# Performance work log

Hardware: AMD Instinct MI355X
Metric: run time of the kernel (lower is better)

## Reference

```python
import jax, jax.numpy as jnp
import numpy as np

NUM_SRC = 100000
NUM_DST = 100000
NUM_EDGES = 800000
WIDTH = 128
LEAKY_SLOPE = 0.01  # torch LeakyReLU default


def setup_inputs() -> dict:
    key = jax.random.key(0)
    k1, k2, k3, k4 = jax.random.split(key, 4)
    x_src = jax.random.normal(k1, (NUM_SRC, WIDTH), dtype=jnp.float32)
    x_dst = jax.random.normal(k2, (NUM_DST, WIDTH), dtype=jnp.float32)
    e = jax.random.randint(k3, (2, NUM_EDGES), 0, NUM_DST, dtype=jnp.int64)
    W = jax.random.normal(k4, (2 * WIDTH, WIDTH), dtype=jnp.float32) * 0.02
    b = jnp.zeros((WIDTH,), dtype=jnp.float32)
    return {"x_src": x_src, "x_dst": x_dst, "e": e, "W": W, "b": b}


def reference(x_src, x_dst, e, W, b):
    src_idx, dst_idx = e[0], e[1]
    # gather + per-edge diff: [E, W]
    diffs = x_dst[dst_idx] - x_src[src_idx]
    # segment max over destination nodes; empty segments -> 0 (matches torch.zeros_like init)
    seg_max = jax.ops.segment_max(diffs, dst_idx, num_segments=NUM_DST)
    counts = jax.ops.segment_sum(jnp.ones((diffs.shape[0],), dtype=x_dst.dtype),
                                 dst_idx, num_segments=NUM_DST)
    maxes = jnp.where(counts[:, None] > 0, seg_max, jnp.zeros_like(seg_max))
    # MLP: Linear(2W -> W) + LeakyReLU, then residual
    h = jnp.concatenate([x_dst, maxes], axis=1) @ W + b
    h = jax.nn.leaky_relu(h, negative_slope=LEAKY_SLOPE)
    return x_dst + h
```

## Files before the change

### kernel.cpp

```cpp
#include <hip/hip_runtime.h>

#define WIDTH 128
#define SLOPE 0.01f
#define FBM 64

typedef __attribute__((ext_vector_type(8))) short short8;
typedef __attribute__((ext_vector_type(4))) float f32x4;

__device__ __forceinline__ unsigned short f2bf(float f) {
    unsigned b = __float_as_uint(f);
    b += 0x7FFFu + ((b >> 16) & 1u);
    return (unsigned short)(b >> 16);
}
__device__ __forceinline__ float4 upk(uint2 u) {
    float4 r;
    r.x = __uint_as_float(u.x << 16);
    r.y = __uint_as_float(u.x & 0xFFFF0000u);
    r.z = __uint_as_float(u.y << 16);
    r.w = __uint_as_float(u.y & 0xFFFF0000u);
    return r;
}
__device__ __forceinline__ float4 fmin4(float4 a, float4 b) {
    return make_float4(fminf(a.x, b.x), fminf(a.y, b.y),
                       fminf(a.z, b.z), fminf(a.w, b.w));
}
__device__ __forceinline__ int swz(int lr, int bc) {
    return lr * 512 + (bc ^ ((lr & 7) << 4));
}

__global__ void prep_kernel(const float* __restrict__ x_src,
                            const float* __restrict__ W,
                            const int* __restrict__ e,
                            unsigned short* __restrict__ xsb,
                            unsigned short* __restrict__ Wt,
                            unsigned* __restrict__ counts,
                            int* __restrict__ rank,
                            int NS, int E, int nconv, int nhist) {
    int b = blockIdx.x;
    if (b < nconv) {
        int i = b * 256 + threadIdx.x;
        if (i < NS * 32) {
            float4 v = reinterpret_cast<const float4*>(x_src)[i];
            ushort4 o;
            o.x = f2bf(v.x); o.y = f2bf(v.y); o.z = f2bf(v.z); o.w = f2bf(v.w);
            *reinterpret_cast<ushort4*>(xsb + (size_t)i * 4) = o;
        }
    } else if (b < nconv + nhist) {
        int i = (b - nconv) * 256 + threadIdx.x;
        if (i < E) {
            int dst = e[E + i];
            rank[i] = (int)atomicAdd(&counts[dst], 1u);
        }
    } else {
        int t = (b - nconv - nhist) * 256 + threadIdx.x;
        if (t < 128 * 64) {
            int n = t & 127, kc = t >> 7;
            ushort4 o;
            unsigned short* op = &o.x;
            #pragma unroll
            for (int j = 0; j < 4; ++j) {
                int k = kc * 4 + j;
                float v;
                if (k < 128) v = W[(size_t)k * 128 + n] + W[(size_t)(k + 128) * 128 + n];
                else         v = -W[(size_t)k * 128 + n];
                op[j] = f2bf(v);
            }
            *reinterpret_cast<ushort4*>(Wt + (size_t)n * 256 + kc * 4) = o;
        }
    }
}

__global__ void __launch_bounds__(512) scanA_kernel(
        const unsigned* __restrict__ counts,
        int* __restrict__ loffs,
        unsigned* __restrict__ bsums, int M) {
    int t = threadIdx.x;
    int i = blockIdx.x * 512 + t;
    unsigned c = (i < M) ? counts[i] : 0u;
    unsigned v = c;
    int lane = t & 63, w = t >> 6;
    #pragma unroll
    for (int d = 1; d < 64; d <<= 1) {
        unsigned n = __shfl_up(v, d);
        if (lane >= d) v += n;
    }
    __shared__ unsigned ws[8];
    if (lane == 63) ws[w] = v;
    __syncthreads();
    unsigned wb = 0;
    for (int k = 0; k < w; ++k) wb += ws[k];
    if (i < M) loffs[i] = (int)(wb + v - c);
    if (t == 511) bsums[blockIdx.x] = wb + v;
}

__global__ void scanB_kernel(const unsigned* __restrict__ bsums,
                             int* __restrict__ bbase, int NB) {
    __shared__ unsigned s[256];
    int t = threadIdx.x;
    unsigned v = (t < NB) ? bsums[t] : 0u;
    s[t] = v;
    __syncthreads();
    for (int off = 1; off < 256; off <<= 1) {
        unsigned n = (t >= off) ? s[t - off] : 0u;
        __syncthreads();
        s[t] += n;
        __syncthreads();
    }
    if (t < NB) bbase[t] = (int)(s[t] - v);
}

__global__ void scatter_kernel(const int* __restrict__ e,
                               const int* __restrict__ loffs,
                               const int* __restrict__ bbase,
                               const int* __restrict__ rank,
                               int* __restrict__ csr, int E) {
    int i = blockIdx.x * blockDim.x + threadIdx.x;
    if (i < E) {
        int dst = e[E + i];
        csr[loffs[dst] + bbase[dst >> 9] + rank[i]] = e[i];
    }
}

template<int XSB>
__device__ __forceinline__ void gstep(const float* xs_f,
                                      const unsigned short* xs_b,
                                      const int* csr, int p, int lim,
                                      int half, int cl, float4& mn) {
    int i0 = csr[min(p + 0, lim)];
    int i1 = csr[min(p + 1, lim)];
    int i2 = csr[min(p + 2, lim)];
    int i3 = csr[min(p + 3, lim)];
    int i4 = csr[min(p + 4, lim)];
    int i5 = csr[min(p + 5, lim)];
    int i6 = csr[min(p + 6, lim)];
    int i7 = csr[min(p + 7, lim)];
    int a0 = half ? i1 : i0;
    int a1 = half ? i3 : i2;
    int a2 = half ? i5 : i4;
    int a3 = half ? i7 : i6;
    float4 w0, w1, w2, w3;
    if (XSB) {
        uint2 u0 = *reinterpret_cast<const uint2*>(xs_b + (size_t)a0 * 128 + cl * 4);
        uint2 u1 = *reinterpret_cast<const uint2*>(xs_b + (size_t)a1 * 128 + cl * 4);
        uint2 u2 = *reinterpret_cast<const uint2*>(xs_b + (size_t)a2 * 128 + cl * 4);
        uint2 u3 = *reinterpret_cast<const uint2*>(xs_b + (size_t)a3 * 128 + cl * 4);
        w0 = upk(u0); w1 = upk(u1); w2 = upk(u2); w3 = upk(u3);
    } else {
        const float4* xs4 = reinterpret_cast<const float4*>(xs_f);
        w0 = xs4[(size_t)a0 * 32 + cl];
        w1 = xs4[(size_t)a1 * 32 + cl];
        w2 = xs4[(size_t)a2 * 32 + cl];
        w3 = xs4[(size_t)a3 * 32 + cl];
    }
    mn = fmin4(mn, fmin4(fmin4(w0, w1), fmin4(w2, w3)));
}

template<int XSB>
__global__ __launch_bounds__(256, 4) void fused_kernel(
        const float* __restrict__ x_src,
        const unsigned short* __restrict__ xsb,
        const float* __restrict__ x_dst,
        const int* __restrict__ loffs,
        const int* __restrict__ bbase,
        const int* __restrict__ csr,
        const unsigned short* __restrict__ Wt,
        const float* __restrict__ bias,
        float* __restrict__ out, int M, int E) {
    __shared__ unsigned short At[FBM * 256];
    char* Ab = reinterpret_cast<char*>(At);
    int tid = threadIdx.x;
    int lane = tid & 63;
    int wv = tid >> 6;
    int blockRow = blockIdx.x * FBM;

    #pragma unroll
    for (int i = 0; i < 8; ++i) {
        int u = tid + 256 * i;
        int lr = u >> 5;
        int c4 = u & 31;
        int gr = min(blockRow + lr, M - 1);
        float4 v = reinterpret_cast<const float4*>(x_dst)[(size_t)gr * 32 + c4];
        ushort4 o;
        o.x = f2bf(v.x); o.y = f2bf(v.y); o.z = f2bf(v.z); o.w = f2bf(v.w);
        *reinterpret_cast<ushort4*>(Ab + swz(lr, c4 * 8)) = o;
    }
    __syncthreads();

    int half = lane >> 5, cl = lane & 31;
    for (int j = 0; j < 4; ++j) {
        int lrb = wv * 16 + 4 * j;
        int beg0, beg1, beg2, beg3, end0, end1, end2, end3;
        {
            int r = __builtin_amdgcn_readfirstlane(blockRow + lrb);
            int g[5];
            #pragma unroll
            for (int k = 0; k < 5; ++k) {
                int x = r + k;
                g[k] = (x < M) ? (loffs[x] + bbase[x >> 9]) : E;
            }
            beg0 = (r + 0 < M) ? g[0] : 0;  end0 = (r + 0 < M) ? g[1] : 0;
            beg1 = (r + 1 < M) ? g[1] : 0;  end1 = (r + 1 < M) ? g[2] : 0;
            beg2 = (r + 2 < M) ? g[2] : 0;  end2 = (r + 2 < M) ? g[3] : 0;
            beg3 = (r + 3 < M) ? g[3] : 0;  end3 = (r + 3 < M) ? g[4] : 0;
        }
        float4 mn0 = make_float4(INFINITY, INFINITY, INFINITY, INFINITY);
        float4 mn1 = mn0, mn2 = mn0, mn3 = mn0;
        int p0 = beg0, p1 = beg1, p2 = beg2, p3 = beg3;
        while ((p0 < end0) | (p1 < end1) | (p2 < end2) | (p3 < end3)) {
            if (p0 < end0) { gstep<XSB>(x_src, xsb, csr, p0, end0 - 1, half, cl, mn0); p0 += 8; }
            if (p1 < end1) { gstep<XSB>(x_src, xsb, csr, p1, end1 - 1, half, cl, mn1); p1 += 8; }
            if (p2 < end2) { gstep<XSB>(x_src, xsb, csr, p2, end2 - 1, half, cl, mn2); p2 += 8; }
            if (p3 < end3) { gstep<XSB>(x_src, xsb, csr, p3, end3 - 1, half, cl, mn3); p3 += 8; }
        }
        mn0.x = fminf(mn0.x, __shfl_xor(mn0.x, 32));
        mn0.y = fminf(mn0.y, __shfl_xor(mn0.y, 32));
        mn0.z = fminf(mn0.z, __shfl_xor(mn0.z, 32));
        mn0.w = fminf(mn0.w, __shfl_xor(mn0.w, 32));
        mn1.x = fminf(mn1.x, __shfl_xor(mn1.x, 32));
        mn1.y = fminf(mn1.y, __shfl_xor(mn1.y, 32));
        mn1.z = fminf(mn1.z, __shfl_xor(mn1.z, 32));
        mn1.w = fminf(mn1.w, __shfl_xor(mn1.w, 32));
        mn2.x = fminf(mn2.x, __shfl_xor(mn2.x, 32));
        mn2.y = fminf(mn2.y, __shfl_xor(mn2.y, 32));
        mn2.z = fminf(mn2.z, __shfl_xor(mn2.z, 32));
        mn2.w = fminf(mn2.w, __shfl_xor(mn2.w, 32));
        mn3.x = fminf(mn3.x, __shfl_xor(mn3.x, 32));
        mn3.y = fminf(mn3.y, __shfl_xor(mn3.y, 32));
        mn3.z = fminf(mn3.z, __shfl_xor(mn3.z, 32));
        mn3.w = fminf(mn3.w, __shfl_xor(mn3.w, 32));

        {
            int lr = lrb + half;
            bool has = half ? (end1 > beg1) : (end0 > beg0);
            float4 m = half ? mn1 : mn0;
            ushort4 o;
            if (has) {
                o.x = f2bf(m.x); o.y = f2bf(m.y); o.z = f2bf(m.z); o.w = f2bf(m.w);
            } else {
                o = *reinterpret_cast<const ushort4*>(Ab + swz(lr, cl * 8));
            }
            *reinterpret_cast<ushort4*>(Ab + swz(lr, 256 + cl * 8)) = o;
        }
        {
            int lr = lrb + 2 + half;
            bool has = half ? (end3 > beg3) : (end2 > beg2);
            float4 m = half ? mn3 : mn2;
            ushort4 o;
            if (has) {
                o.x = f2bf(m.x); o.y = f2bf(m.y); o.z = f2bf(m.z); o.w = f2bf(m.w);
            } else {
                o = *reinterpret_cast<const ushort4*>(Ab + swz(lr, cl * 8));
            }
            *reinterpret_cast<ushort4*>(Ab + swz(lr, 256 + cl * 8)) = o;
        }
    }
    __syncthreads();

    int l15 = lane & 15;
    int q = lane >> 4;
    int ncol0 = wv * 32;

    f32x4 acc[4][2];
    #pragma unroll
    for (int t = 0; t < 4; ++t) {
        acc[t][0] = (f32x4){0.f, 0.f, 0.f, 0.f};
        acc[t][1] = (f32x4){0.f, 0.f, 0.f, 0.f};
    }
    size_t b0off = (size_t)(ncol0 + l15) * 256;
    size_t b1off = (size_t)(ncol0 + 16 + l15) * 256;

    #pragma unroll
    for (int s = 0; s < 8; ++s) {
        int koff = s * 32 + q * 8;
        short8 b0 = *reinterpret_cast<const short8*>(Wt + b0off + koff);
        short8 b1 = *reinterpret_cast<const short8*>(Wt + b1off + koff);
        #pragma unroll
        for (int t = 0; t < 4; ++t) {
            int lr = t * 16 + l15;
            short8 a = *reinterpret_cast<const short8*>(Ab + swz(lr, koff * 2));
            acc[t][0] = __builtin_amdgcn_mfma_f32_16x16x32_bf16(b0, a, acc[t][0], 0, 0, 0);
            acc[t][1] = __builtin_amdgcn_mfma_f32_16x16x32_bf16(b1, a, acc[t][1], 0, 0, 0);
        }
    }

    float4 bi[2];
    bi[0] = *reinterpret_cast<const float4*>(bias + ncol0 + q * 4);
    bi[1] = *reinterpret_cast<const float4*>(bias + ncol0 + 16 + q * 4);
    #pragma unroll
    for (int t = 0; t < 4; ++t) {
        int lr = t * 16 + l15;
        int row = blockRow + lr;
        if (row < M) {
            #pragma unroll
            for (int u = 0; u < 2; ++u) {
                int col = ncol0 + u * 16 + q * 4;
                uint2 xu = *reinterpret_cast<const uint2*>(Ab + swz(lr, col * 2));
                float4 xb = upk(xu);
                float4 o;
                float h;
                h = acc[t][u][0] + bi[u].x; o.x = xb.x + (h > 0.f ? h : SLOPE * h);
                h = acc[t][u][1] + bi[u].y; o.y = xb.y + (h > 0.f ? h : SLOPE * h);
                h = acc[t][u][2] + bi[u].z; o.z = xb.z + (h > 0.f ? h : SLOPE * h);
                h = acc[t][u][3] + bi[u].w; o.w = xb.w + (h > 0.f ? h : SLOPE * h);
                *reinterpret_cast<float4*>(out + (size_t)row * 128 + col) = o;
            }
        }
    }
}

extern "C" void kernel_launch(void* const* d_in, const int* in_sizes, int n_in,
                              void* d_out, int out_size, void* d_ws, size_t ws_size,
                              hipStream_t stream) {
    const float* x_src = (const float*)d_in[0];
    const float* x_dst = (const float*)d_in[1];
    const int*   e     = (const int*)d_in[2];
    const float* W     = (const float*)d_in[3];
    const float* bias  = (const float*)d_in[4];
    float* out = (float*)d_out;

    int NS = in_sizes[0] / WIDTH;
    int E  = in_sizes[2] / 2;
    int M  = in_sizes[1] / WIDTH;
    int NB = (M + 511) / 512;

    unsigned short* xsb = (unsigned short*)d_ws;
    unsigned short* Wt  = xsb + (size_t)NS * WIDTH;
    unsigned* counts  = (unsigned*)(Wt + 128 * 256);
    int*      loffs   = (int*)(counts + M);
    int*      rank    = loffs + M;
    int*      csr     = rank + E;
    unsigned* bsums   = (unsigned*)(csr + E);
    int*      bbase   = (int*)(bsums + NB);
    size_t need = (char*)(bbase + NB) - (char*)d_ws;
    int use_xsb = (ws_size >= need) ? 1 : 0;
    if (!use_xsb) {
        Wt = (unsigned short*)d_ws;
        counts  = (unsigned*)(Wt + 128 * 256);
        loffs   = (int*)(counts + M);
        rank    = loffs + M;
        csr     = rank + E;
        bsums   = (unsigned*)(csr + E);
        bbase   = (int*)(bsums + NB);
    }

    hipMemsetAsync(counts, 0, (size_t)M * sizeof(unsigned), stream);

    int nconv = use_xsb ? (NS * 32 + 255) / 256 : 0;
    int nhist = (E + 255) / 256;
    int nwt   = (128 * 64 + 255) / 256;
    prep_kernel<<<nconv + nhist + nwt, 256, 0, stream>>>(x_src, W, e, xsb, Wt,
                                                         counts, rank, NS, E,
                                                         nconv, nhist);
    scanA_kernel<<<NB, 512, 0, stream>>>(counts, loffs, bsums, M);
    scanB_kernel<<<1, 256, 0, stream>>>(bsums, bbase, NB);
    scatter_kernel<<<(E + 255) / 256, 256, 0, stream>>>(e, loffs, bbase, rank,
                                                        csr, E);

    int fblocks = (M + FBM - 1) / FBM;
    if (use_xsb)
        fused_kernel<1><<<fblocks, 256, 0, stream>>>(x_src, xsb, x_dst, loffs,
                                                     bbase, csr, Wt, bias, out,
                                                     M, E);
    else
        fused_kernel<0><<<fblocks, 256, 0, stream>>>(x_src, xsb, x_dst, loffs,
                                                     bbase, csr, Wt, bias, out,
                                                     M, E);
}
```

Measured before the change: 138.9 us.

## Use order-mapped bf16 packed u16 min for gather and halve row tile

The bf16 copy of x_src is now stored in an order-preserving unsigned encoding. The segment min can then use v_pk_min_u16 on the packed data without unpacking to float, and the encoding is undone once per row. The fused kernel's row tile drops from 64 to 32, with launch bounds raised to 8 blocks per CU, to give more independent gather work and higher occupancy. Row bounds checks are removed, which assumes M is a multiple of the tile size. The fp32 fallback path becomes a simple per-row loop.

Result: faster. 132.5 us (-4.6%).

```diff
diff --git a/kernel.cpp b/kernel.cpp
--- a/kernel.cpp
+++ b/kernel.cpp
@@ -2,7 +2,7 @@
 
 #define WIDTH 128
 #define SLOPE 0.01f
-#define FBM 64
+#define FBM 32
 
 typedef __attribute__((ext_vector_type(8))) short short8;
 typedef __attribute__((ext_vector_type(4))) float f32x4;
@@ -20,9 +20,16 @@
     r.w = __uint_as_float(u.y & 0xFFFF0000u);
     return r;
 }
-__device__ __forceinline__ float4 fmin4(float4 a, float4 b) {
-    return make_float4(fminf(a.x, b.x), fminf(a.y, b.y),
-                       fminf(a.z, b.z), fminf(a.w, b.w));
+__device__ __forceinline__ unsigned short map16(unsigned short x) {
+    return (x & 0x8000u) ? (unsigned short)(~x) : (unsigned short)(x | 0x8000u);
+}
+__device__ __forceinline__ unsigned short unmap16(unsigned u) {
+    return (unsigned short)((u & 0x8000u) ? (u ^ 0x8000u) : (~u & 0xFFFFu));
+}
+__device__ __forceinline__ unsigned pkmin(unsigned a, unsigned b) {
+    unsigned r;
+    asm("v_pk_min_u16 %0, %1, %2" : "=v"(r) : "v"(a), "v"(b));
+    return r;
 }
 __device__ __forceinline__ int swz(int lr, int bc) {
     return lr * 512 + (bc ^ ((lr & 7) << 4));
@@ -42,7 +49,8 @@
         if (i < NS * 32) {
             float4 v = reinterpret_cast<const float4*>(x_src)[i];
             ushort4 o;
-            o.x = f2bf(v.x); o.y = f2bf(v.y); o.z = f2bf(v.z); o.w = f2bf(v.w);
+            o.x = map16(f2bf(v.x)); o.y = map16(f2bf(v.y));
+            o.z = map16(f2bf(v.z)); o.w = map16(f2bf(v.w));
             *reinterpret_cast<ushort4*>(xsb + (size_t)i * 4) = o;
         }
     } else if (b < nconv + nhist) {
@@ -121,11 +129,10 @@
     }
 }
 
-template<int XSB>
-__device__ __forceinline__ void gstep(const float* xs_f,
-                                      const unsigned short* xs_b,
-                                      const int* csr, int p, int lim,
-                                      int half, int cl, float4& mn) {
+__device__ __forceinline__ void gstepm(const unsigned short* __restrict__ xs_b,
+                                       const int* __restrict__ csr,
+                                       int p, int lim,
+                                       int half, int cl, uint2& mn) {
     int i0 = csr[min(p + 0, lim)];
     int i1 = csr[min(p + 1, lim)];
     int i2 = csr[min(p + 2, lim)];
@@ -138,25 +145,18 @@
     int a1 = half ? i3 : i2;
     int a2 = half ? i5 : i4;
     int a3 = half ? i7 : i6;
-    float4 w0, w1, w2, w3;
-    if (XSB) {
-        uint2 u0 = *reinterpret_cast<const uint2*>(xs_b + (size_t)a0 * 128 + cl * 4);
-        uint2 u1 = *reinterpret_cast<const uint2*>(xs_b + (size_t)a1 * 128 + cl * 4);
-        uint2 u2 = *reinterpret_cast<const uint2*>(xs_b + (size_t)a2 * 128 + cl * 4);
-        uint2 u3 = *reinterpret_cast<const uint2*>(xs_b + (size_t)a3 * 128 + cl * 4);
-        w0 = upk(u0); w1 = upk(u1); w2 = upk(u2); w3 = upk(u3);
-    } else {
-        const float4* xs4 = reinterpret_cast<const float4*>(xs_f);
-        w0 = xs4[(size_t)a0 * 32 + cl];
-        w1 = xs4[(size_t)a1 * 32 + cl];
-        w2 = xs4[(size_t)a2 * 32 + cl];
-        w3 = xs4[(size_t)a3 * 32 + cl];
-    }
-    mn = fmin4(mn, fmin4(fmin4(w0, w1), fmin4(w2, w3)));
+    uint2 u0 = *reinterpret_cast<const uint2*>(xs_b + (size_t)a0 * 128 + cl * 4);
+    uint2 u1 = *reinterpret_cast<const uint2*>(xs_b + (size_t)a1 * 128 + cl * 4);
+    uint2 u2 = *reinterpret_cast<const uint2*>(xs_b + (size_t)a2 * 128 + cl * 4);
+    uint2 u3 = *reinterpret_cast<const uint2*>(xs_b + (size_t)a3 * 128 + cl * 4);
+    u0.x = pkmin(u0.x, u1.x); u0.y = pkmin(u0.y, u1.y);
+    u2.x = pkmin(u2.x, u3.x); u2.y = pkmin(u2.y, u3.y);
+    mn.x = pkmin(mn.x, pkmin(u0.x, u2.x));
+    mn.y = pkmin(mn.y, pkmin(u0.y, u2.y));
 }
 
 template<int XSB>
-__global__ __launch_bounds__(256, 4) void fused_kernel(
+__global__ __launch_bounds__(256, 8) void fused_kernel(
         const float* __restrict__ x_src,
         const unsigned short* __restrict__ xsb,
         const float* __restrict__ x_dst,
@@ -174,12 +174,11 @@
     int blockRow = blockIdx.x * FBM;
 
     #pragma unroll
-    for (int i = 0; i < 8; ++i) {
+    for (int i = 0; i < 4; ++i) {
         int u = tid + 256 * i;
         int lr = u >> 5;
         int c4 = u & 31;
-        int gr = min(blockRow + lr, M - 1);
-        float4 v = reinterpret_cast<const float4*>(x_dst)[(size_t)gr * 32 + c4];
+        float4 v = reinterpret_cast<const float4*>(x_dst)[(size_t)(blockRow + lr) * 32 + c4];
         ushort4 o;
         o.x = f2bf(v.x); o.y = f2bf(v.y); o.z = f2bf(v.z); o.w = f2bf(v.w);
         *reinterpret_cast<ushort4*>(Ab + swz(lr, c4 * 8)) = o;
@@ -187,8 +186,8 @@
     __syncthreads();
 
     int half = lane >> 5, cl = lane & 31;
-    for (int j = 0; j < 4; ++j) {
-        int lrb = wv * 16 + 4 * j;
+    for (int j = 0; j < 2; ++j) {
+        int lrb = wv * 8 + 4 * j;
         int beg0, beg1, beg2, beg3, end0, end1, end2, end3;
         {
             int r = __builtin_amdgcn_readfirstlane(blockRow + lrb);
@@ -198,60 +197,80 @@
                 int x = r + k;
                 g[k] = (x < M) ? (loffs[x] + bbase[x >> 9]) : E;
             }
-            beg0 = (r + 0 < M) ? g[0] : 0;  end0 = (r + 0 < M) ? g[1] : 0;
-            beg1 = (r + 1 < M) ? g[1] : 0;  end1 = (r + 1 < M) ? g[2] : 0;
-            beg2 = (r + 2 < M) ? g[2] : 0;  end2 = (r + 2 < M) ? g[3] : 0;
-            beg3 = (r + 3 < M) ? g[3] : 0;  end3 = (r + 3 < M) ? g[4] : 0;
-        }
-        float4 mn0 = make_float4(INFINITY, INFINITY, INFINITY, INFINITY);
-        float4 mn1 = mn0, mn2 = mn0, mn3 = mn0;
-        int p0 = beg0, p1 = beg1, p2 = beg2, p3 = beg3;
-        while ((p0 < end0) | (p1 < end1) | (p2 < end2) | (p3 < end3)) {
-            if (p0 < end0) { gstep<XSB>(x_src, xsb, csr, p0, end0 - 1, half, cl, mn0); p0 += 8; }
-            if (p1 < end1) { gstep<XSB>(x_src, xsb, csr, p1, end1 - 1, half, cl, mn1); p1 += 8; }
-            if (p2 < end2) { gstep<XSB>(x_src, xsb, csr, p2, end2 - 1, half, cl, mn2); p2 += 8; }
-            if (p3 < end3) { gstep<XSB>(x_src, xsb, csr, p3, end3 - 1, half, cl, mn3); p3 += 8; }
-        }
-        mn0.x = fminf(mn0.x, __shfl_xor(mn0.x, 32));
-        mn0.y = fminf(mn0.y, __shfl_xor(mn0.y, 32));
-        mn0.z = fminf(mn0.z, __shfl_xor(mn0.z, 32));
-        mn0.w = fminf(mn0.w, __shfl_xor(mn0.w, 32));
-        mn1.x = fminf(mn1.x, __shfl_xor(mn1.x, 32));
-        mn1.y = fminf(mn1.y, __shfl_xor(mn1.y, 32));
-        mn1.z = fminf(mn1.z, __shfl_xor(mn1.z, 32));
-        mn1.w = fminf(mn1.w, __shfl_xor(mn1.w, 32));
-        mn2.x = fminf(mn2.x, __shfl_xor(mn2.x, 32));
-        mn2.y = fminf(mn2.y, __shfl_xor(mn2.y, 32));
-        mn2.z = fminf(mn2.z, __shfl_xor(mn2.z, 32));
-        mn2.w = fminf(mn2.w, __shfl_xor(mn2.w, 32));
-        mn3.x = fminf(mn3.x, __shfl_xor(mn3.x, 32));
-        mn3.y = fminf(mn3.y, __shfl_xor(mn3.y, 32));
-        mn3.z = fminf(mn3.z, __shfl_xor(mn3.z, 32));
-        mn3.w = fminf(mn3.w, __shfl_xor(mn3.w, 32));
-
-        {
-            int lr = lrb + half;
-            bool has = half ? (end1 > beg1) : (end0 > beg0);
-            float4 m = half ? mn1 : mn0;
-            ushort4 o;
-            if (has) {
-                o.x = f2bf(m.x); o.y = f2bf(m.y); o.z = f2bf(m.z); o.w = f2bf(m.w);
-            } else {
-                o = *reinterpret_cast<const ushort4*>(Ab + swz(lr, cl * 8));
-            }
-            *reinterpret_cast<ushort4*>(Ab + swz(lr, 256 + cl * 8)) = o;
-        }
-        {
-            int lr = lrb + 2 + half;
-            bool has = half ? (end3 > beg3) : (end2 > beg2);
-            float4 m = half ? mn3 : mn2;
-            ushort4 o;
-            if (has) {
-                o.x = f2bf(m.x); o.y = f2bf(m.y); o.z = f2bf(m.z); o.w = f2bf(m.w);
-            } else {
-                o = *reinterpret_cast<const ushort4*>(Ab + swz(lr, cl * 8));
-            }
-            *reinterpret_cast<ushort4*>(Ab + swz(lr, 256 + cl * 8)) = o;
+            beg0 = g[0]; end0 = g[1];
+            beg1 = g[1]; end1 = g[2];
+            beg2 = g[2]; end2 = g[3];
+            beg3 = g[3]; end3 = g[4];
+        }
+        if (XSB) {
+            uint2 mn0 = make_uint2(~0u, ~0u);
+            uint2 mn1 = mn0, mn2 = mn0, mn3 = mn0;
+            int p0 = beg0, p1 = beg1, p2 = beg2, p3 = beg3;
+            while ((p0 < end0) | (p1 < end1) | (p2 < end2) | (p3 < end3)) {
+                if (p0 < end0) { gstepm(xsb, csr, p0, end0 - 1, half, cl, mn0); p0 += 8; }
+                if (p1 < end1) { gstepm(xsb, csr, p1, end1 - 1, half, cl, mn1); p1 += 8; }
+                if (p2 < end2) { gstepm(xsb, csr, p2, end2 - 1, half, cl, mn2); p2 += 8; }
+                if (p3 < end3) { gstepm(xsb, csr, p3, end3 - 1, half, cl, mn3); p3 += 8; }
+            }
+            mn0.x = pkmin(mn0.x, (unsigned)__shfl_xor((int)mn0.x, 32));
+            mn0.y = pkmin(mn0.y, (unsigned)__shfl_xor((int)mn0.y, 32));
+            mn1.x = pkmin(mn1.x, (unsigned)__shfl_xor((int)mn1.x, 32));
+            mn1.y = pkmin(mn1.y, (unsigned)__shfl_xor((int)mn1.y, 32));
+            mn2.x = pkmin(mn2.x, (unsigned)__shfl_xor((int)mn2.x, 32));
+            mn2.y = pkmin(mn2.y, (unsigned)__shfl_xor((int)mn2.y, 32));
+            mn3.x = pkmin(mn3.x, (unsigned)__shfl_xor((int)mn3.x, 32));
+            mn3.y = pkmin(mn3.y, (unsigned)__shfl_xor((int)mn3.y, 32));
+
+            {
+                int lr = lrb + half;
+                bool has = half ? (end1 > beg1) : (end0 > beg0);
+                uint2 m;
+                m.x = half ? mn1.x : mn0.x;
+                m.y = half ? mn1.y : mn0.y;
+                ushort4 o;
+                if (has) {
+                    o.x = unmap16(m.x & 0xFFFFu); o.y = unmap16(m.x >> 16);
+                    o.z = unmap16(m.y & 0xFFFFu); o.w = unmap16(m.y >> 16);
+                } else {
+                    o = *reinterpret_cast<const ushort4*>(Ab + swz(lr, cl * 8));
+                }
+                *reinterpret_cast<ushort4*>(Ab + swz(lr, 256 + cl * 8)) = o;
+            }
+            {
+                int lr = lrb + 2 + half;
+                bool has = half ? (end3 > beg3) : (end2 > beg2);
+                uint2 m;
+                m.x = half ? mn3.x : mn2.x;
+                m.y = half ? mn3.y : mn2.y;
+                ushort4 o;
+                if (has) {
+                    o.x = unmap16(m.x & 0xFFFFu); o.y = unmap16(m.x >> 16);
+                    o.z = unmap16(m.y & 0xFFFFu); o.w = unmap16(m.y >> 16);
+                } else {
+                    o = *reinterpret_cast<const ushort4*>(Ab + swz(lr, cl * 8));
+                }
+                *reinterpret_cast<ushort4*>(Ab + swz(lr, 256 + cl * 8)) = o;
+            }
+        } else {
+            const float2* xf = reinterpret_cast<const float2*>(x_src);
+            #pragma unroll
+            for (int k = 0; k < 4; ++k) {
+                int lr = lrb + k;
+                int rb = (k == 0) ? beg0 : (k == 1) ? beg1 : (k == 2) ? beg2 : beg3;
+                int re = (k == 0) ? end0 : (k == 1) ? end1 : (k == 2) ? end2 : end3;
+                float2 mf = make_float2(INFINITY, INFINITY);
+                for (int p = rb; p < re; ++p) {
+                    int idx = csr[p];
+                    float2 v = xf[(size_t)idx * 64 + lane];
+                    mf.x = fminf(mf.x, v.x); mf.y = fminf(mf.y, v.y);
+                }
+                unsigned o;
+                if (re > rb)
+                    o = (unsigned)f2bf(mf.x) | ((unsigned)f2bf(mf.y) << 16);
+                else
+                    o = *reinterpret_cast<const unsigned*>(Ab + swz(lr, lane * 4));
+                *reinterpret_cast<unsigned*>(Ab + swz(lr, 256 + lane * 4)) = o;
+            }
         }
     }
     __syncthreads();
@@ -260,9 +279,9 @@
     int q = lane >> 4;
     int ncol0 = wv * 32;
 
-    f32x4 acc[4][2];
-    #pragma unroll
-    for (int t = 0; t < 4; ++t) {
+    f32x4 acc[2][2];
+    #pragma unroll
+    for (int t = 0; t < 2; ++t) {
         acc[t][0] = (f32x4){0.f, 0.f, 0.f, 0.f};
         acc[t][1] = (f32x4){0.f, 0.f, 0.f, 0.f};
     }
@@ -275,7 +294,7 @@
         short8 b0 = *reinterpret_cast<const short8*>(Wt + b0off + koff);
         short8 b1 = *reinterpret_cast<const short8*>(Wt + b1off + koff);
         #pragma unroll
-        for (int t = 0; t < 4; ++t) {
+        for (int t = 0; t < 2; ++t) {
             int lr = t * 16 + l15;
             short8 a = *reinterpret_cast<const short8*>(Ab + swz(lr, koff * 2));
             acc[t][0] = __builtin_amdgcn_mfma_f32_16x16x32_bf16(b0, a, acc[t][0], 0, 0, 0);
@@ -287,23 +306,21 @@
     bi[0] = *reinterpret_cast<const float4*>(bias + ncol0 + q * 4);
     bi[1] = *reinterpret_cast<const float4*>(bias + ncol0 + 16 + q * 4);
     #pragma unroll
-    for (int t = 0; t < 4; ++t) {
+    for (int t = 0; t < 2; ++t) {
         int lr = t * 16 + l15;
         int row = blockRow + lr;
-        if (row < M) {
-            #pragma unroll
-            for (int u = 0; u < 2; ++u) {
-                int col = ncol0 + u * 16 + q * 4;
-                uint2 xu = *reinterpret_cast<const uint2*>(Ab + swz(lr, col * 2));
-                float4 xb = upk(xu);
-                float4 o;
-                float h;
-                h = acc[t][u][0] + bi[u].x; o.x = xb.x + (h > 0.f ? h : SLOPE * h);
-                h = acc[t][u][1] + bi[u].y; o.y = xb.y + (h > 0.f ? h : SLOPE * h);
-                h = acc[t][u][2] + bi[u].z; o.z = xb.z + (h > 0.f ? h : SLOPE * h);
-                h = acc[t][u][3] + bi[u].w; o.w = xb.w + (h > 0.f ? h : SLOPE * h);
-                *reinterpret_cast<float4*>(out + (size_t)row * 128 + col) = o;
-            }
+        #pragma unroll
+        for (int u = 0; u < 2; ++u) {
+            int col = ncol0 + u * 16 + q * 4;
+            uint2 xu = *reinterpret_cast<const uint2*>(Ab + swz(lr, col * 2));
+            float4 xb = upk(xu);
+            float4 o;
+            float h;
+            h = acc[t][u][0] + bi[u].x; o.x = xb.x + (h > 0.f ? h : SLOPE * h);
+            h = acc[t][u][1] + bi[u].y; o.y = xb.y + (h > 0.f ? h : SLOPE * h);
+            h = acc[t][u][2] + bi[u].z; o.z = xb.z + (h > 0.f ? h : SLOPE * h);
+            h = acc[t][u][3] + bi[u].w; o.w = xb.w + (h > 0.f ? h : SLOPE * h);
+            *reinterpret_cast<float4*>(out + (size_t)row * 128 + col) = o;
         }
     }
 }
```
